# Performance work log

Hardware: AMD Instinct MI355X
Metric: run time of the kernel (lower is better)

The kernel has to match this reference:

```python
import jax, jax.numpy as jnp
import numpy as np
import math

D_MODEL = 1024
NUM_HEAD = 16


def setup_inputs() -> dict:
    key = jax.random.key(0)
    k1, k2, k3, k4, k5 = jax.random.split(key, 5)
    B, S, D = 4, 2048, D_MODEL
    lim = 1.0 / math.sqrt(D)
    x = jax.random.normal(k1, (B, S, D), dtype=jnp.float32)
    Wqkv = jax.random.uniform(k2, (D, D), jnp.float32, -lim, lim)
    bqkv = jax.random.uniform(k3, (D,), jnp.float32, -lim, lim)
    Wo = jax.random.uniform(k4, (D, D), jnp.float32, -lim, lim)
    bo = jax.random.uniform(k5, (D,), jnp.float32, -lim, lim)
    return {"x": x, "Wqkv": Wqkv, "bqkv": bqkv, "Wo": Wo, "bo": bo}


def reference(x, Wqkv, bqkv, Wo, bo):
    B, S, D = x.shape
    H = NUM_HEAD
    dk = D // H
    # Single shared linear for Q, K, V (qkv_fc applied to x for all three)
    proj = jnp.einsum('bsd,de->bse', x, Wqkv) + bqkv  # [B,S,D]
    # Faithful to source: raw view(B, H, -1, dk) -- reinterprets memory,
    # NOT a head transpose.
    q = proj.reshape(B, H, S, dk)
    k = q
    v = q
    scores = jnp.einsum('bhqd,bhkd->bhqk', q, k) / math.sqrt(dk)  # [B,H,S,S]
    attn = jax.nn.softmax(scores, axis=-1)
    feats = jnp.einsum('bhqk,bhkd->bhqd', attn, v)  # [B,H,S,dk]
    # transpose(1,2) then view(B, -1, H*dk)
    merged = feats.transpose(0, 2, 1, 3).reshape(B, S, H * dk)
    out = jnp.einsum('bsd,de->bse', merged, Wo) + bo
    return out
```

## Files before the change

kernel.cpp:

```cpp
#include <hip/hip_runtime.h>
#include <hip/hip_bf16.h>

typedef __bf16 bf16;
typedef __attribute__((ext_vector_type(8))) __bf16 bf16x8;
typedef __attribute__((ext_vector_type(4))) float f32x4;
typedef __attribute__((ext_vector_type(16))) float f32x16;
typedef __attribute__((ext_vector_type(4))) unsigned short u16x4;

#define MFMA_BF16(a, b, c) __builtin_amdgcn_mfma_f32_16x16x32_bf16((a), (b), (c), 0, 0, 0)
#define MFMA32(a, b, c) __builtin_amdgcn_mfma_f32_32x32x16_bf16((a), (b), (c), 0, 0, 0)
#define EXP2F(x) __builtin_amdgcn_exp2f(x)

__device__ __forceinline__ void gload_lds16(const bf16* g, bf16* l) {
  __builtin_amdgcn_global_load_lds(
      (__attribute__((address_space(1))) void*)(g),
      (__attribute__((address_space(3))) void*)(l), 16, 0, 0);
}

__device__ __forceinline__ int cvtpk(float lo, float hi) {
  int r;
  asm("v_cvt_pk_bf16_f32 %0, %1, %2" : "=v"(r) : "v"(lo), "v"(hi));
  return r;
}
__device__ __forceinline__ void plswap(int& a, int& b) {
  asm volatile("v_permlane32_swap_b32 %0, %1" : "+v"(a), "+v"(b));
}
__device__ __forceinline__ float swap_max(float x) {
  int u = __float_as_int(x), v;
  asm volatile("v_mov_b32 %0, %1" : "=v"(v) : "v"(u));
  plswap(u, v);
  return fmaxf(__int_as_float(u), __int_as_float(v));
}
__device__ __forceinline__ float swap_add(float x) {
  int u = __float_as_int(x), v;
  asm volatile("v_mov_b32 %0, %1" : "=v"(v) : "v"(u));
  plswap(u, v);
  return __int_as_float(u) + __int_as_float(v);
}

__global__ void transcvt2(const float* __restrict__ W0, bf16* __restrict__ T0,
                          const float* __restrict__ W1, bf16* __restrict__ T1) {
  const float* src = blockIdx.z ? W1 : W0;
  bf16* dst = blockIdx.z ? T1 : T0;
  __shared__ float t[32][33];
  const int bx = blockIdx.x * 32, by = blockIdx.y * 32;
  const int tx = threadIdx.x, ty = threadIdx.y;
#pragma unroll
  for (int i = 0; i < 4; ++i)
    t[ty + i * 8][tx] = src[(long)(by + ty + i * 8) * 1024 + bx + tx];
  __syncthreads();
#pragma unroll
  for (int i = 0; i < 4; ++i)
    dst[(long)(bx + ty + i * 8) * 1024 + by + tx] = (bf16)t[tx][ty + i * 8];
}

template <bool A_IS_F32, bool OUT_F32>
__global__ __launch_bounds__(256) void gemm_bt(const void* __restrict__ Av,
                                               const bf16* __restrict__ Bt,
                                               const float* __restrict__ bias,
                                               void* __restrict__ Cv) {
  __shared__ __align__(16) bf16 As[128 * 32];
  __shared__ __align__(16) bf16 Bs[128 * 32];
  const int tid = threadIdx.x;
  const int l = tid & 63, w = tid >> 6;
  const int wr = w >> 1, wc = w & 1;
  const int lo = l & 15, g = l >> 4;
  const int m0 = blockIdx.x * 128;
  const int n0 = blockIdx.y * 128;
  const bf16* Ab = (const bf16*)Av + (long)m0 * 1024;
  const float* Af = (const float*)Av + (long)m0 * 1024;
  const bf16* Bb = Bt + (long)n0 * 1024;
  const int srow = tid >> 2;
  const int schunk = (tid & 3) * 8;
  f32x4 acc[4][4] = {};
  for (int k0 = 0; k0 < 1024; k0 += 32) {
    __syncthreads();
    if constexpr (A_IS_F32) {
#pragma unroll
      for (int h = 0; h < 2; ++h) {
        const float* p = Af + (long)(srow + h * 64) * 1024 + k0 + schunk;
        f32x4 u0 = *(const f32x4*)p;
        f32x4 u1 = *(const f32x4*)(p + 4);
        bf16x8 vv;
#pragma unroll
        for (int e = 0; e < 4; ++e) {
          vv[e] = (bf16)u0[e];
          vv[4 + e] = (bf16)u1[e];
        }
        *(bf16x8*)&As[h * 2048 + tid * 8] = vv;
      }
    } else {
      gload_lds16(Ab + (long)srow * 1024 + k0 + schunk, As + tid * 8);
      gload_lds16(Ab + (long)(srow + 64) * 1024 + k0 + schunk, As + 2048 + tid * 8);
    }
    gload_lds16(Bb + (long)srow * 1024 + k0 + schunk, Bs + tid * 8);
    gload_lds16(Bb + (long)(srow + 64) * 1024 + k0 + schunk, Bs + 2048 + tid * 8);
    __syncthreads();
    bf16x8 af[4], bfr[4];
#pragma unroll
    for (int m = 0; m < 4; ++m)
      af[m] = *(const bf16x8*)&As[(wr * 64 + m * 16 + lo) * 32 + g * 8];
#pragma unroll
    for (int n = 0; n < 4; ++n)
      bfr[n] = *(const bf16x8*)&Bs[(wc * 64 + n * 16 + lo) * 32 + g * 8];
#pragma unroll
    for (int m = 0; m < 4; ++m)
#pragma unroll
      for (int n = 0; n < 4; ++n)
        acc[m][n] = MFMA_BF16(af[m], bfr[n], acc[m][n]);
  }
#pragma unroll
  for (int n = 0; n < 4; ++n) {
    const int col = n0 + wc * 64 + n * 16 + lo;
    const float bv = bias[col];
#pragma unroll
    for (int m = 0; m < 4; ++m) {
      const long row0 = m0 + wr * 64 + m * 16 + g * 4;
#pragma unroll
      for (int j = 0; j < 4; ++j) {
        if constexpr (OUT_F32)
          ((float*)Cv)[(row0 + j) * 1024 + col] = acc[m][n][j] + bv;
        else
          ((bf16*)Cv)[(row0 + j) * 1024 + col] = (bf16)(acc[m][n][j] + bv);
      }
    }
  }
}

__global__ __launch_bounds__(256) void attn(const bf16* __restrict__ proj,
                                            bf16* __restrict__ merged) {
  __shared__ __align__(16) bf16 Vt[2][64][34];
  const int bid = blockIdx.x;
  const int qb = bid & 15;
  const int hh = (bid >> 4) & 15;
  const int b = bid >> 8;
  const bf16* P = proj + (long)b * 2097152 + (long)hh * 131072;
  const int tid = threadIdx.x;
  const int w = tid >> 6, l = tid & 63;
  const int l31 = l & 31;
  const int hf = l >> 5;
  const int qrow = qb * 128 + w * 32;

  const int kvp = tid >> 4;
  const int dc = tid & 15;
  int* VtI = (int*)Vt;

  int pu = l, pv;
  asm volatile("v_mov_b32 %0, %1" : "=v"(pv) : "v"(pu));
  plswap(pu, pv);
  const bool dir1 = (__shfl(pu, 33, 64) == 1);

  const float QSCALE = 0.125f * 1.44269504088896f;
  bf16x8 qf[4];
#pragma unroll
  for (int s = 0; s < 4; ++s) {
    bf16x8 t = *(const bf16x8*)&P[(long)(qrow + l31) * 64 + s * 16 + hf * 8];
#pragma unroll
    for (int e = 0; e < 8; ++e) t[e] = (bf16)((float)t[e] * QSCALE);
    qf[s] = t;
  }

  f32x16 o0 = {}, o1 = {};
  float mq = -1e30f, lq = 0.f;

  bf16x8 kA[4], kB[4];
  {
    u16x4 v0 = *(const u16x4*)&P[(long)(2 * kvp) * 64 + dc * 4];
    u16x4 v1 = *(const u16x4*)&P[(long)(2 * kvp + 1) * 64 + dc * 4];
#pragma unroll
    for (int dd = 0; dd < 4; ++dd)
      VtI[(dc * 4 + dd) * 17 + kvp] = ((int)v0[dd]) | (((int)v1[dd]) << 16);
  }
#pragma unroll
  for (int s = 0; s < 4; ++s)
    kA[s] = *(const bf16x8*)&P[(long)l31 * 64 + s * 16 + hf * 8];
  __syncthreads();

  for (int t2 = 0; t2 < 32; ++t2) {
#pragma unroll
    for (int ph = 0; ph < 2; ++ph) {
      const int t = t2 * 2 + ph;
      const int tn = (t < 63) ? t + 1 : 63;
      u16x4 vn0 = *(const u16x4*)&P[((long)tn * 32 + 2 * kvp) * 64 + dc * 4];
      u16x4 vn1 = *(const u16x4*)&P[((long)tn * 32 + 2 * kvp + 1) * 64 + dc * 4];
      f32x16 s;
      if (ph == 0) {
        s = MFMA32(kA[0], qf[0], f32x16{});
        s = MFMA32(kA[1], qf[1], s);
        s = MFMA32(kA[2], qf[2], s);
        s = MFMA32(kA[3], qf[3], s);
      } else {
        s = MFMA32(kB[0], qf[0], f32x16{});
        s = MFMA32(kB[1], qf[1], s);
        s = MFMA32(kB[2], qf[2], s);
        s = MFMA32(kB[3], qf[3], s);
      }
#pragma unroll
      for (int sx = 0; sx < 4; ++sx) {
        bf16x8 kv8 = *(const bf16x8*)&P[((long)tn * 32 + l31) * 64 + sx * 16 + hf * 8];
        if (ph == 0) kB[sx] = kv8; else kA[sx] = kv8;
      }
      float mx = s[0];
#pragma unroll
      for (int i = 1; i < 16; ++i) mx = fmaxf(mx, s[i]);
      mx = swap_max(mx);
      if (__any(mx > mq)) {
        const float mnew = fmaxf(mq, mx);
        const float corr = EXP2F(mq - mnew);
        mq = mnew;
        lq *= corr;
#pragma unroll
        for (int i = 0; i < 16; ++i) { o0[i] *= corr; o1[i] *= corr; }
      }
      float ps = 0.f;
#pragma unroll
      for (int i = 0; i < 16; ++i) {
        const float p = EXP2F(s[i] - mq);
        s[i] = p;
        ps += p;
      }
      ps = swap_add(ps);
      lq += ps;
      int p0 = cvtpk(s[0], s[1]), p1 = cvtpk(s[2], s[3]);
      int p2 = cvtpk(s[4], s[5]), p3 = cvtpk(s[6], s[7]);
      int p4 = cvtpk(s[8], s[9]), p5 = cvtpk(s[10], s[11]);
      int p6 = cvtpk(s[12], s[13]), p7 = cvtpk(s[14], s[15]);
      if (dir1) {
        plswap(p0, p2); plswap(p1, p3); plswap(p4, p6); plswap(p5, p7);
      } else {
        plswap(p2, p0); plswap(p3, p1); plswap(p6, p4); plswap(p7, p5);
      }
      int bi0[4] = {p0, p1, p2, p3};
      int bi1[4] = {p4, p5, p6, p7};
      bf16x8 pb0 = *(bf16x8*)bi0;
      bf16x8 pb1 = *(bf16x8*)bi1;
      {
        bf16x8 va;
        va = *(const bf16x8*)&Vt[ph][l31][hf * 8];
        o0 = MFMA32(va, pb0, o0);
        va = *(const bf16x8*)&Vt[ph][l31][16 + hf * 8];
        o0 = MFMA32(va, pb1, o0);
        va = *(const bf16x8*)&Vt[ph][32 + l31][hf * 8];
        o1 = MFMA32(va, pb0, o1);
        va = *(const bf16x8*)&Vt[ph][32 + l31][16 + hf * 8];
        o1 = MFMA32(va, pb1, o1);
      }
      {
        int* W = VtI + (ph ^ 1) * (64 * 17);
#pragma unroll
        for (int dd = 0; dd < 4; ++dd)
          W[(dc * 4 + dd) * 17 + kvp] = ((int)vn0[dd]) | (((int)vn1[dd]) << 16);
      }
      __syncthreads();
    }
  }

  const float inv = 1.0f / lq;
  bf16* mb = merged + (long)b * 2097152 + hh * 64;
  const long rowoff = (long)(qrow + l31) * 1024;
  const int dbase[8] = {0, 2, 8, 10, 16, 18, 24, 26};
#pragma unroll
  for (int r = 0; r < 8; ++r) {
    const int d = dbase[r] + 4 * hf;
    *(int*)&mb[rowoff + d] = cvtpk(o0[2 * r] * inv, o0[2 * r + 1] * inv);
    *(int*)&mb[rowoff + 32 + d] = cvtpk(o1[2 * r] * inv, o1[2 * r + 1] * inv);
  }
}

extern "C" void kernel_launch(void* const* d_in, const int* in_sizes, int n_in,
                              void* d_out, int out_size, void* d_ws, size_t ws_size,
                              hipStream_t stream) {
  const float* x = (const float*)d_in[0];
  const float* Wqkv = (const float*)d_in[1];
  const float* bqkv = (const float*)d_in[2];
  const float* Wo = (const float*)d_in[3];
  const float* bo = (const float*)d_in[4];
  float* out = (float*)d_out;

  char* ws = (char*)d_ws;
  bf16* proj = (bf16*)(ws);
  bf16* merged = (bf16*)(ws + 16777216);
  bf16* WqkvT = (bf16*)(ws + 33554432);
  bf16* WoT = (bf16*)(ws + 35651584);

  transcvt2<<<dim3(32, 32, 2), dim3(32, 8), 0, stream>>>(Wqkv, WqkvT, Wo, WoT);
  gemm_bt<true, false><<<dim3(64, 8), dim3(256), 0, stream>>>(x, WqkvT, bqkv, proj);
  attn<<<dim3(1024), dim3(256), 0, stream>>>(proj, merged);
  gemm_bt<false, true><<<dim3(64, 8), dim3(256), 0, stream>>>(merged, WoT, bo, out);
}
```

Before: 326.8 us.

## Pre-convert x to bf16, widen GEMM K-tile with swizzled LDS, tune attention loop

A separate kernel now converts x to bf16, so both projection GEMMs take the global-to-LDS direct-load path. The GEMM K-tile grows from 32 to 64 and uses an XOR-swizzled LDS layout to cut bank conflicts. The attention loop splits the QK^T MFMA chain into two independent accumulators and raises wave priority around the MFMAs. It also uses tree reductions for the max and sum, and rescales the online softmax only when the new max exceeds the running one by more than 8 (in log2 units). The lazy rescale lets exp2 values reach up to 2^8 before rescaling, which could affect bf16 precision, and the extra conversion kernel adds a pass over x.

```diff
diff --git a/kernel.cpp b/kernel.cpp
--- a/kernel.cpp
+++ b/kernel.cpp
@@ -54,60 +54,67 @@
     dst[(long)(bx + ty + i * 8) * 1024 + by + tx] = (bf16)t[tx][ty + i * 8];
 }
 
-template <bool A_IS_F32, bool OUT_F32>
-__global__ __launch_bounds__(256) void gemm_bt(const void* __restrict__ Av,
+__global__ __launch_bounds__(256) void cvtx(const float* __restrict__ x,
+                                            bf16* __restrict__ xb) {
+  const long i = ((long)blockIdx.x * 256 + threadIdx.x) * 8;
+  f32x4 u0 = *(const f32x4*)&x[i];
+  f32x4 u1 = *(const f32x4*)&x[i + 4];
+  bf16x8 v;
+#pragma unroll
+  for (int e = 0; e < 4; ++e) {
+    v[e] = (bf16)u0[e];
+    v[4 + e] = (bf16)u1[e];
+  }
+  *(bf16x8*)&xb[i] = v;
+}
+
+template <bool OUT_F32>
+__global__ __launch_bounds__(256) void gemm_bt(const bf16* __restrict__ A,
                                                const bf16* __restrict__ Bt,
                                                const float* __restrict__ bias,
                                                void* __restrict__ Cv) {
-  __shared__ __align__(16) bf16 As[128 * 32];
-  __shared__ __align__(16) bf16 Bs[128 * 32];
+  __shared__ __align__(16) bf16 As[128 * 64];
+  __shared__ __align__(16) bf16 Bs[128 * 64];
   const int tid = threadIdx.x;
   const int l = tid & 63, w = tid >> 6;
   const int wr = w >> 1, wc = w & 1;
   const int lo = l & 15, g = l >> 4;
   const int m0 = blockIdx.x * 128;
   const int n0 = blockIdx.y * 128;
-  const bf16* Ab = (const bf16*)Av + (long)m0 * 1024;
-  const float* Af = (const float*)Av + (long)m0 * 1024;
-  const bf16* Bb = Bt + (long)n0 * 1024;
-  const int srow = tid >> 2;
-  const int schunk = (tid & 3) * 8;
+  const int srow = tid >> 3;
+  const int sc = tid & 7;
   f32x4 acc[4][4] = {};
-  for (int k0 = 0; k0 < 1024; k0 += 32) {
+  for (int k0 = 0; k0 < 1024; k0 += 64) {
     __syncthreads();
-    if constexpr (A_IS_F32) {
-#pragma unroll
-      for (int h = 0; h < 2; ++h) {
-        const float* p = Af + (long)(srow + h * 64) * 1024 + k0 + schunk;
-        f32x4 u0 = *(const f32x4*)p;
-        f32x4 u1 = *(const f32x4*)(p + 4);
-        bf16x8 vv;
-#pragma unroll
-        for (int e = 0; e < 4; ++e) {
-          vv[e] = (bf16)u0[e];
-          vv[4 + e] = (bf16)u1[e];
-        }
-        *(bf16x8*)&As[h * 2048 + tid * 8] = vv;
-      }
-    } else {
-      gload_lds16(Ab + (long)srow * 1024 + k0 + schunk, As + tid * 8);
-      gload_lds16(Ab + (long)(srow + 64) * 1024 + k0 + schunk, As + 2048 + tid * 8);
+#pragma unroll
+    for (int h = 0; h < 4; ++h) {
+      const int r = srow + h * 32;
+      const int swc = (sc ^ (r & 7)) * 8;
+      gload_lds16(A + (long)(m0 + r) * 1024 + k0 + swc, As + h * 2048 + tid * 8);
+      gload_lds16(Bt + (long)(n0 + r) * 1024 + k0 + swc, Bs + h * 2048 + tid * 8);
     }
-    gload_lds16(Bb + (long)srow * 1024 + k0 + schunk, Bs + tid * 8);
-    gload_lds16(Bb + (long)(srow + 64) * 1024 + k0 + schunk, Bs + 2048 + tid * 8);
     __syncthreads();
-    bf16x8 af[4], bfr[4];
-#pragma unroll
-    for (int m = 0; m < 4; ++m)
-      af[m] = *(const bf16x8*)&As[(wr * 64 + m * 16 + lo) * 32 + g * 8];
-#pragma unroll
-    for (int n = 0; n < 4; ++n)
-      bfr[n] = *(const bf16x8*)&Bs[(wc * 64 + n * 16 + lo) * 32 + g * 8];
-#pragma unroll
-    for (int m = 0; m < 4; ++m)
-#pragma unroll
-      for (int n = 0; n < 4; ++n)
-        acc[m][n] = MFMA_BF16(af[m], bfr[n], acc[m][n]);
+    bf16x8 af[2][4], bfr[2][4];
+#pragma unroll
+    for (int kk = 0; kk < 2; ++kk) {
+#pragma unroll
+      for (int m = 0; m < 4; ++m) {
+        const int R = wr * 64 + m * 16 + lo;
+        af[kk][m] = *(const bf16x8*)&As[R * 64 + (((kk * 4 + g) ^ (R & 7)) * 8)];
+      }
+#pragma unroll
+      for (int n = 0; n < 4; ++n) {
+        const int R = wc * 64 + n * 16 + lo;
+        bfr[kk][n] = *(const bf16x8*)&Bs[R * 64 + (((kk * 4 + g) ^ (R & 7)) * 8)];
+      }
+    }
+#pragma unroll
+    for (int kk = 0; kk < 2; ++kk)
+#pragma unroll
+      for (int m = 0; m < 4; ++m)
+#pragma unroll
+        for (int n = 0; n < 4; ++n)
+          acc[m][n] = MFMA_BF16(af[kk][m], bfr[kk][n], acc[m][n]);
   }
 #pragma unroll
   for (int n = 0; n < 4; ++n) {
@@ -183,28 +190,35 @@
       const int tn = (t < 63) ? t + 1 : 63;
       u16x4 vn0 = *(const u16x4*)&P[((long)tn * 32 + 2 * kvp) * 64 + dc * 4];
       u16x4 vn1 = *(const u16x4*)&P[((long)tn * 32 + 2 * kvp + 1) * 64 + dc * 4];
-      f32x16 s;
+      f32x16 sa, sb;
+      __builtin_amdgcn_s_setprio(1);
       if (ph == 0) {
-        s = MFMA32(kA[0], qf[0], f32x16{});
-        s = MFMA32(kA[1], qf[1], s);
-        s = MFMA32(kA[2], qf[2], s);
-        s = MFMA32(kA[3], qf[3], s);
+        sa = MFMA32(kA[0], qf[0], f32x16{});
+        sb = MFMA32(kA[1], qf[1], f32x16{});
+        sa = MFMA32(kA[2], qf[2], sa);
+        sb = MFMA32(kA[3], qf[3], sb);
       } else {
-        s = MFMA32(kB[0], qf[0], f32x16{});
-        s = MFMA32(kB[1], qf[1], s);
-        s = MFMA32(kB[2], qf[2], s);
-        s = MFMA32(kB[3], qf[3], s);
-      }
+        sa = MFMA32(kB[0], qf[0], f32x16{});
+        sb = MFMA32(kB[1], qf[1], f32x16{});
+        sa = MFMA32(kB[2], qf[2], sa);
+        sb = MFMA32(kB[3], qf[3], sb);
+      }
+      __builtin_amdgcn_s_setprio(0);
 #pragma unroll
       for (int sx = 0; sx < 4; ++sx) {
         bf16x8 kv8 = *(const bf16x8*)&P[((long)tn * 32 + l31) * 64 + sx * 16 + hf * 8];
         if (ph == 0) kB[sx] = kv8; else kA[sx] = kv8;
       }
-      float mx = s[0];
-#pragma unroll
-      for (int i = 1; i < 16; ++i) mx = fmaxf(mx, s[i]);
+      f32x16 s;
+#pragma unroll
+      for (int i = 0; i < 16; ++i) s[i] = sa[i] + sb[i];
+      float q0 = fmaxf(fmaxf(s[0], s[1]), fmaxf(s[2], s[3]));
+      float q1 = fmaxf(fmaxf(s[4], s[5]), fmaxf(s[6], s[7]));
+      float q2 = fmaxf(fmaxf(s[8], s[9]), fmaxf(s[10], s[11]));
+      float q3 = fmaxf(fmaxf(s[12], s[13]), fmaxf(s[14], s[15]));
+      float mx = fmaxf(fmaxf(q0, q1), fmaxf(q2, q3));
       mx = swap_max(mx);
-      if (__any(mx > mq)) {
+      if (!__all(mx <= mq + 8.f)) {
         const float mnew = fmaxf(mq, mx);
         const float corr = EXP2F(mq - mnew);
         mq = mnew;
@@ -212,15 +226,16 @@
 #pragma unroll
         for (int i = 0; i < 16; ++i) { o0[i] *= corr; o1[i] *= corr; }
       }
-      float ps = 0.f;
-#pragma unroll
-      for (int i = 0; i < 16; ++i) {
-        const float p = EXP2F(s[i] - mq);
-        s[i] = p;
-        ps += p;
-      }
-      ps = swap_add(ps);
-      lq += ps;
+#pragma unroll
+      for (int i = 0; i < 16; ++i) s[i] = EXP2F(s[i] - mq);
+      {
+        float a0 = s[0] + s[1], a1 = s[2] + s[3], a2 = s[4] + s[5], a3 = s[6] + s[7];
+        float a4 = s[8] + s[9], a5 = s[10] + s[11], a6 = s[12] + s[13], a7 = s[14] + s[15];
+        float b0 = a0 + a1, b1 = a2 + a3, b2 = a4 + a5, b3 = a6 + a7;
+        float ps = (b0 + b1) + (b2 + b3);
+        ps = swap_add(ps);
+        lq += ps;
+      }
       int p0 = cvtpk(s[0], s[1]), p1 = cvtpk(s[2], s[3]);
       int p2 = cvtpk(s[4], s[5]), p3 = cvtpk(s[6], s[7]);
       int p4 = cvtpk(s[8], s[9]), p5 = cvtpk(s[10], s[11]);
@@ -235,15 +250,16 @@
       bf16x8 pb0 = *(bf16x8*)bi0;
       bf16x8 pb1 = *(bf16x8*)bi1;
       {
-        bf16x8 va;
-        va = *(const bf16x8*)&Vt[ph][l31][hf * 8];
-        o0 = MFMA32(va, pb0, o0);
-        va = *(const bf16x8*)&Vt[ph][l31][16 + hf * 8];
-        o0 = MFMA32(va, pb1, o0);
-        va = *(const bf16x8*)&Vt[ph][32 + l31][hf * 8];
-        o1 = MFMA32(va, pb0, o1);
-        va = *(const bf16x8*)&Vt[ph][32 + l31][16 + hf * 8];
-        o1 = MFMA32(va, pb1, o1);
+        bf16x8 va0 = *(const bf16x8*)&Vt[ph][l31][hf * 8];
+        bf16x8 va1 = *(const bf16x8*)&Vt[ph][l31][16 + hf * 8];
+        bf16x8 va2 = *(const bf16x8*)&Vt[ph][32 + l31][hf * 8];
+        bf16x8 va3 = *(const bf16x8*)&Vt[ph][32 + l31][16 + hf * 8];
+        __builtin_amdgcn_s_setprio(1);
+        o0 = MFMA32(va0, pb0, o0);
+        o1 = MFMA32(va2, pb0, o1);
+        o0 = MFMA32(va1, pb1, o0);
+        o1 = MFMA32(va3, pb1, o1);
+        __builtin_amdgcn_s_setprio(0);
       }
       {
         int* W = VtI + (ph ^ 1) * (64 * 17);
@@ -280,11 +296,13 @@
   char* ws = (char*)d_ws;
   bf16* proj = (bf16*)(ws);
   bf16* merged = (bf16*)(ws + 16777216);
+  bf16* xb = (bf16*)(ws + 16777216);
   bf16* WqkvT = (bf16*)(ws + 33554432);
   bf16* WoT = (bf16*)(ws + 35651584);
 
   transcvt2<<<dim3(32, 32, 2), dim3(32, 8), 0, stream>>>(Wqkv, WqkvT, Wo, WoT);
-  gemm_bt<true, false><<<dim3(64, 8), dim3(256), 0, stream>>>(x, WqkvT, bqkv, proj);
+  cvtx<<<dim3(4096), dim3(256), 0, stream>>>(x, xb);
+  gemm_bt<false><<<dim3(64, 8), dim3(256), 0, stream>>>(xb, WqkvT, bqkv, proj);
   attn<<<dim3(1024), dim3(256), 0, stream>>>(proj, merged);
-  gemm_bt<false, true><<<dim3(64, 8), dim3(256), 0, stream>>>(merged, WoT, bo, out);
-}
+  gemm_bt<true><<<dim3(64, 8), dim3(256), 0, stream>>>(merged, WoT, bo, out);
+}
```

Result: faster. 309.2 us (-5.4%).
